# Optimization experiments

Measured on AMD Instinct MI355X. Metric: run time of the kernel, lower is better.

Reference implementation:

```python
import jax, jax.numpy as jnp
import numpy as np

H = 64; H2 = 32; B = 256; NPART = 64
NP = B * NPART          # 16384 part nodes
PER_TF = 512            # torque/force nodes per graph
NT = B * PER_TF; NF = NT
E = 262144              # edges per edge type
L = 5; T = 4            # 4 main hetero layers + 1 actor layer; 4 edge types
NEG = 0.2; EPS = 1e-5


def _seg_softmax(e, seg, n):
    # softmax over entries sharing the same segment id (along axis 0)
    m = jax.lax.stop_gradient(jax.ops.segment_max(e, seg, num_segments=n))
    ex = jnp.exp(e - m[seg])
    s = jax.ops.segment_sum(ex, seg, num_segments=n)
    return ex / s[seg]


def _gat(x_s, x_d, es, ed, Ws, Wd, a_s, a_d, b, n_dst):
    # PyG GATConv, heads=1, add_self_loops=False, bipartite (x_src, x_dst)
    hs = x_s @ Ws                      # [Ns,H]
    hd = x_d @ Wd                      # [Nd,H]
    e = jax.nn.leaky_relu((hs @ a_s)[es] + (hd @ a_d)[ed], NEG)   # [E]
    al = _seg_softmax(e, ed, n_dst)                                # attn per dst neighborhood
    return jax.ops.segment_sum(al[:, None] * hs[es], ed, num_segments=n_dst) + b


def _hetero_layer(xp, xt, xf, edges, Ws, Wd, a_s, a_d, b):
    # to_hetero(aggr='sum'): one GATConv per edge type, sum into each dst type
    (pts, ptd), (tps, tpd), (pfs, pfd), (fps, fpd) = edges
    out_t = _gat(xp, xt, pts, ptd, Ws[0], Wd[0], a_s[0], a_d[0], b[0], xt.shape[0])
    out_p = (_gat(xt, xp, tps, tpd, Ws[1], Wd[1], a_s[1], a_d[1], b[1], xp.shape[0])
             + _gat(xf, xp, fps, fpd, Ws[3], Wd[3], a_s[3], a_d[3], b[3], xp.shape[0]))
    out_f = _gat(xp, xf, pfs, pfd, Ws[2], Wd[2], a_s[2], a_d[2], b[2], xf.shape[0])
    return out_p, out_t, out_f


def _pool(x):
    # MultiAggregation([max, min, mean]); segments are uniform -> reshape
    xr = x.reshape(B, -1, x.shape[-1])
    return jnp.concatenate([xr.max(1), xr.min(1), xr.mean(1)], axis=-1)


def reference(mass, part_state, torque_x, force_x,
              e_pt_src, e_pt_dst, e_tp_src, e_tp_dst,
              e_pf_src, e_pf_dst, e_fp_src, e_fp_dst,
              batch, part_id,
              emb_parts_W, emb_state, W_src, W_dst, a_src, a_dst, b_conv,
              ln_gamma, ln_beta, out_a_W, out_a_b,
              innet_W, innet_b, full_W, full_b, outnet_W, outnet_b):
    edges = ((e_pt_src, e_pt_dst), (e_tp_src, e_tp_dst),
             (e_pf_src, e_pf_dst), (e_fp_src, e_fp_dst))
    idx = part_state[:, 0] + 2 * part_state[:, 1]
    xp = jnp.concatenate([mass @ emb_parts_W, emb_state[idx]], axis=-1)  # [NP,H]
    xt, xf = torque_x, force_x
    for l in range(4):  # main hetero GAT, ReLU between layers, none after last
        xp, xt, xf = _hetero_layer(xp, xt, xf, edges,
                                   W_src[l], W_dst[l], a_src[l], a_dst[l], b_conv[l])
        if l < 3:
            xp, xt, xf = jax.nn.relu(xp), jax.nn.relu(xt), jax.nn.relu(xf)
    # actor: 1-layer hetero GAT (no activation)
    ap, at, af = _hetero_layer(xp, xt, xf, edges,
                               W_src[4], W_dst[4], a_src[4], a_dst[4], b_conv[4])
    # node LayerNorm
    mu = ap.mean(-1, keepdims=True)
    var = ((ap - mu) ** 2).mean(-1, keepdims=True)
    ra = (ap - mu) / jnp.sqrt(var + EPS) * ln_gamma + ln_beta
    ra = ra @ out_a_W + out_a_b                         # [NP,2]
    soft = _seg_softmax(ra, batch, B)                   # softmax per graph, per channel
    actions = jnp.zeros((B, 2, NPART), dtype=ra.dtype).at[batch, :, part_id].set(soft)
    actions = actions.reshape(B, 2 * NPART)
    rep = jnp.concatenate([_pool(xp), _pool(xt), _pool(xf)], axis=1)   # [B, 9H]
    repV = jax.nn.gelu(rep @ innet_W + innet_b, approximate=False)
    repV = jax.nn.gelu(repV @ full_W + full_b, approximate=False)
    V = jnp.tanh(repV @ outnet_W + outnet_b)            # [B,1]
    return actions, V


def setup_inputs():
    key = jax.random.key(0)
    ks = iter(jax.random.split(key, 40))
    f32 = jnp.float32
    inp = {}
    inp['mass'] = jax.random.uniform(next(ks), (NP, 1), dtype=f32)
    inp['part_state'] = jax.random.randint(next(ks), (NP, 2), 0, 2, dtype=jnp.int32)
    inp['torque_x'] = jax.random.normal(next(ks), (NT, H), dtype=f32)
    inp['force_x'] = jax.random.normal(next(ks), (NF, H), dtype=f32)
    for name, n in [('e_pt_src', NP), ('e_pt_dst', NT), ('e_tp_src', NT), ('e_tp_dst', NP),
                    ('e_pf_src', NP), ('e_pf_dst', NF), ('e_fp_src', NF), ('e_fp_dst', NP)]:
        inp[name] = jax.random.randint(next(ks), (E,), 0, n, dtype=jnp.int32)
    inp['batch'] = (jnp.arange(NP) // NPART).astype(jnp.int32)
    inp['part_id'] = (jnp.arange(NP) % NPART).astype(jnp.int32)
    s = 1.0 / np.sqrt(H)
    inp['emb_parts_W'] = jax.random.normal(next(ks), (1, H2), dtype=f32)
    inp['emb_state'] = jax.random.normal(next(ks), (4, H2), dtype=f32)
    inp['W_src'] = jax.random.normal(next(ks), (L, T, H, H), dtype=f32) * s
    inp['W_dst'] = jax.random.normal(next(ks), (L, T, H, H), dtype=f32) * s
    inp['a_src'] = jax.random.normal(next(ks), (L, T, H), dtype=f32) * s
    inp['a_dst'] = jax.random.normal(next(ks), (L, T, H), dtype=f32) * s
    inp['b_conv'] = jax.random.normal(next(ks), (L, T, H), dtype=f32) * 0.01
    inp['ln_gamma'] = jnp.ones((H,), dtype=f32)
    inp['ln_beta'] = jnp.zeros((H,), dtype=f32)
    inp['out_a_W'] = jax.random.normal(next(ks), (H, 2), dtype=f32) * s
    inp['out_a_b'] = jnp.zeros((2,), dtype=f32)
    inp['innet_W'] = jax.random.normal(next(ks), (9 * H, H), dtype=f32) / np.sqrt(9.0 * H)
    inp['innet_b'] = jnp.zeros((H,), dtype=f32)
    inp['full_W'] = jax.random.normal(next(ks), (H, H), dtype=f32) * s
    inp['full_b'] = jnp.zeros((H,), dtype=f32)
    inp['outnet_W'] = jax.random.normal(next(ks), (H, 1), dtype=f32) * s
    inp['outnet_b'] = jnp.zeros((1,), dtype=f32)
    return inp
```

## Files before the change

kernel.cpp:

```cpp
#include <hip/hip_runtime.h>
#include <math.h>

#define NP_ 16384
#define NT_ 131072
#define NF_ 131072
#define E_  262144
#define B_  256
#define NDTOT 294912
#define E4_  1048576

#define D0 0
#define D1 131072
#define D2 147456
#define D3 278528
#define S0 0
#define S1 16384
#define S2 147456
#define S3 163840

__device__ __forceinline__ float dot4(float4 a, float4 b) {
  return a.x * b.x + a.y * b.y + a.z * b.z + a.w * b.w;
}

__device__ __forceinline__ void gather2(
    int kb0, int ke0, float ad0, const float* __restrict__ aS0, const float* __restrict__ x0,
    int kb1, int ke1, float ad1, const float* __restrict__ aS1, const float* __restrict__ x1,
    const int* __restrict__ sortsrc, int q, int lanebase,
    float4* __restrict__ acc0o, float* __restrict__ si0o,
    float4* __restrict__ acc1o, float* __restrict__ si1o) {
  float4 acc0 = make_float4(0.f, 0.f, 0.f, 0.f);
  float4 acc1 = make_float4(0.f, 0.f, 0.f, 0.f);
  float m0 = -3e38f, m1 = -3e38f, sum0 = 0.f, sum1 = 0.f;
  int len = max(ke0 - kb0, ke1 - kb1);
  for (int c = 0; c < len; c += 16) {
    int k0 = kb0 + c + q, k1 = kb1 + c + q;
    int v0 = k0 < ke0, v1 = k1 < ke1;
    int sx0 = v0 ? sortsrc[k0] : 0;
    int sx1 = v1 ? sortsrc[k1] : 0;
    float e0 = -3e38f, e1 = -3e38f;
    if (v0) { float t = aS0[sx0] + ad0; e0 = t > 0.f ? t : 0.2f * t; }
    if (v1) { float t = aS1[sx1] + ad1; e1 = t > 0.f ? t : 0.2f * t; }
    float cm0 = e0, cm1 = e1;
#pragma unroll
    for (int off = 1; off < 16; off <<= 1) {
      cm0 = fmaxf(cm0, __shfl_xor(cm0, off));
      cm1 = fmaxf(cm1, __shfl_xor(cm1, off));
    }
    float mn0 = fmaxf(m0, cm0), mn1 = fmaxf(m1, cm1);
    float w0 = v0 ? __expf(e0 - mn0) : 0.f;
    float w1 = v1 ? __expf(e1 - mn1) : 0.f;
    float ws0 = w0, ws1 = w1;
#pragma unroll
    for (int off = 1; off < 16; off <<= 1) {
      ws0 += __shfl_xor(ws0, off);
      ws1 += __shfl_xor(ws1, off);
    }
    float r0 = __expf(m0 - mn0), r1 = __expf(m1 - mn1);
    sum0 = sum0 * r0 + ws0;
    sum1 = sum1 * r1 + ws1;
    acc0.x *= r0; acc0.y *= r0; acc0.z *= r0; acc0.w *= r0;
    acc1.x *= r1; acc1.y *= r1; acc1.z *= r1; acc1.w *= r1;
    int cnt0 = ke0 - (kb0 + c); cnt0 = cnt0 < 0 ? 0 : (cnt0 > 16 ? 16 : cnt0);
    int cnt1 = ke1 - (kb1 + c); cnt1 = cnt1 < 0 ? 0 : (cnt1 > 16 ? 16 : cnt1);
    int cmax = max(cnt0, cnt1);
    for (int i = 0; i < cmax; i += 4) {
      float wa0 = __shfl(w0, lanebase + i, 64);
      float wa1 = __shfl(w0, lanebase + i + 1, 64);
      float wa2 = __shfl(w0, lanebase + i + 2, 64);
      float wa3 = __shfl(w0, lanebase + i + 3, 64);
      int sa0 = __shfl(sx0, lanebase + i, 64);
      int sa1 = __shfl(sx0, lanebase + i + 1, 64);
      int sa2 = __shfl(sx0, lanebase + i + 2, 64);
      int sa3 = __shfl(sx0, lanebase + i + 3, 64);
      float wb0 = __shfl(w1, lanebase + i, 64);
      float wb1 = __shfl(w1, lanebase + i + 1, 64);
      float wb2 = __shfl(w1, lanebase + i + 2, 64);
      float wb3 = __shfl(w1, lanebase + i + 3, 64);
      int sb0 = __shfl(sx1, lanebase + i, 64);
      int sb1 = __shfl(sx1, lanebase + i + 1, 64);
      int sb2 = __shfl(sx1, lanebase + i + 2, 64);
      int sb3 = __shfl(sx1, lanebase + i + 3, 64);
      float4 xa0 = *(const float4*)(x0 + (size_t)sa0 * 64 + q * 4);
      float4 xa1 = *(const float4*)(x0 + (size_t)sa1 * 64 + q * 4);
      float4 xa2 = *(const float4*)(x0 + (size_t)sa2 * 64 + q * 4);
      float4 xa3 = *(const float4*)(x0 + (size_t)sa3 * 64 + q * 4);
      float4 xb0 = *(const float4*)(x1 + (size_t)sb0 * 64 + q * 4);
      float4 xb1 = *(const float4*)(x1 + (size_t)sb1 * 64 + q * 4);
      float4 xb2 = *(const float4*)(x1 + (size_t)sb2 * 64 + q * 4);
      float4 xb3 = *(const float4*)(x1 + (size_t)sb3 * 64 + q * 4);
      acc0.x += wa0 * xa0.x + wa1 * xa1.x + wa2 * xa2.x + wa3 * xa3.x;
      acc0.y += wa0 * xa0.y + wa1 * xa1.y + wa2 * xa2.y + wa3 * xa3.y;
      acc0.z += wa0 * xa0.z + wa1 * xa1.z + wa2 * xa2.z + wa3 * xa3.z;
      acc0.w += wa0 * xa0.w + wa1 * xa1.w + wa2 * xa2.w + wa3 * xa3.w;
      acc1.x += wb0 * xb0.x + wb1 * xb1.x + wb2 * xb2.x + wb3 * xb3.x;
      acc1.y += wb0 * xb0.y + wb1 * xb1.y + wb2 * xb2.y + wb3 * xb3.y;
      acc1.z += wb0 * xb0.z + wb1 * xb1.z + wb2 * xb2.z + wb3 * xb3.z;
      acc1.w += wb0 * xb0.w + wb1 * xb1.w + wb2 * xb2.w + wb3 * xb3.w;
    }
    m0 = mn0; m1 = mn1;
  }
  *si0o = (sum0 > 0.f) ? 1.f / sum0 : 0.f;
  *si1o = (sum1 > 0.f) ? 1.f / sum1 : 0.f;
  *acc0o = acc0;
  *acc1o = acc1;
}

__device__ __forceinline__ void gather4(
    int kbA, int keA, float adA,
    int kbB, int keB, float adB,
    int kbC, int keC, float adC,
    int kbD, int keD, float adD,
    const float* __restrict__ aS, const float* __restrict__ x,
    const int* __restrict__ sortsrc, int q, int lanebase,
    float4* accAo, float* siAo, float4* accBo, float* siBo,
    float4* accCo, float* siCo, float4* accDo, float* siDo) {
  float4 aA = make_float4(0.f, 0.f, 0.f, 0.f);
  float4 aB = aA, aC = aA, aDv = aA;
  float mA = -3e38f, mB = -3e38f, mC = -3e38f, mD = -3e38f;
  float sA = 0.f, sB = 0.f, sC = 0.f, sD = 0.f;
  int len = max(max(keA - kbA, keB - kbB), max(keC - kbC, keD - kbD));
  for (int c = 0; c < len; c += 16) {
    int kA = kbA + c + q, kB = kbB + c + q, kC = kbC + c + q, kD = kbD + c + q;
    int vA = kA < keA, vB = kB < keB, vC = kC < keC, vD = kD < keD;
    int iA = vA ? sortsrc[kA] : 0;
    int iB = vB ? sortsrc[kB] : 0;
    int iC = vC ? sortsrc[kC] : 0;
    int iD = vD ? sortsrc[kD] : 0;
    float eA = -3e38f, eB = -3e38f, eC = -3e38f, eD = -3e38f;
    if (vA) { float u = aS[iA] + adA; eA = u > 0.f ? u : 0.2f * u; }
    if (vB) { float u = aS[iB] + adB; eB = u > 0.f ? u : 0.2f * u; }
    if (vC) { float u = aS[iC] + adC; eC = u > 0.f ? u : 0.2f * u; }
    if (vD) { float u = aS[iD] + adD; eD = u > 0.f ? u : 0.2f * u; }
    float cA = eA, cB = eB, cC = eC, cD = eD;
#pragma unroll
    for (int off = 1; off < 16; off <<= 1) {
      cA = fmaxf(cA, __shfl_xor(cA, off));
      cB = fmaxf(cB, __shfl_xor(cB, off));
      cC = fmaxf(cC, __shfl_xor(cC, off));
      cD = fmaxf(cD, __shfl_xor(cD, off));
    }
    float nA = fmaxf(mA, cA), nB = fmaxf(mB, cB);
    float nC = fmaxf(mC, cC), nD = fmaxf(mD, cD);
    float wA = vA ? __expf(eA - nA) : 0.f;
    float wB = vB ? __expf(eB - nB) : 0.f;
    float wC = vC ? __expf(eC - nC) : 0.f;
    float wD = vD ? __expf(eD - nD) : 0.f;
    float uA = wA, uB = wB, uC = wC, uD = wD;
#pragma unroll
    for (int off = 1; off < 16; off <<= 1) {
      uA += __shfl_xor(uA, off);
      uB += __shfl_xor(uB, off);
      uC += __shfl_xor(uC, off);
      uD += __shfl_xor(uD, off);
    }
    float rA = __expf(mA - nA), rB = __expf(mB - nB);
    float rC = __expf(mC - nC), rD = __expf(mD - nD);
    sA = sA * rA + uA; sB = sB * rB + uB;
// ... 280 lines not shown
    pos = atomicAdd(&cur[d.z >> sh], 1); pairs[pos] = make_int2(d.z, s.z);
    pos = atomicAdd(&cur[d.w >> sh], 1); pairs[pos] = make_int2(d.w, s.w);
  }
}

__global__ __launch_bounds__(256) void k_build(const int2* __restrict__ pairs,
    const int* __restrict__ granBase, int* __restrict__ rowptr,
    int* __restrict__ sortsrc) {
  __shared__ int cnt[2048];
  __shared__ int psum[256];
  int g = blockIdx.x;
  int t = g >> 6, gg = g & 63;
  int rows = (t & 1) ? 256 : 2048;
  int rowLo = gg * rows;
  int csr0;
  if (t == 0) csr0 = D0 + rowLo;
  else if (t == 1) csr0 = D1 + rowLo;
  else if (t == 2) csr0 = D2 + rowLo;
  else csr0 = D3 + rowLo;
  int eb = granBase[g], ee = granBase[g + 1];
  int tid = threadIdx.x;
  for (int i = tid; i < rows; i += 256) cnt[i] = 0;
  __syncthreads();
  for (int i = eb + tid; i < ee; i += 256) {
    int2 p = pairs[i];
    atomicAdd(&cnt[p.x - rowLo], 1);
  }
  __syncthreads();
  int per = rows >> 8;
  int b0 = tid * per;
  int s = 0;
  for (int j = 0; j < per; j++) s += cnt[b0 + j];
  psum[tid] = s;
  __syncthreads();
  for (int off = 1; off < 256; off <<= 1) {
    int x = 0; if (tid >= off) x = psum[tid - off];
    __syncthreads(); psum[tid] += x; __syncthreads();
  }
  int run = psum[tid] - s;
  for (int j = 0; j < per; j++) {
    int v = cnt[b0 + j];
    cnt[b0 + j] = run;
    rowptr[csr0 + b0 + j] = eb + run;
    run += v;
  }
  __syncthreads();
  for (int i = eb + tid; i < ee; i += 256) {
    int2 p = pairs[i];
    int pos = eb + atomicAdd(&cnt[p.x - rowLo], 1);
    sortsrc[pos] = p.y;
  }
}

__global__ __launch_bounds__(256) void k_part(int l,
    const float* __restrict__ Wsrc, const float* __restrict__ bconv,
    const float* __restrict__ xt, const float* __restrict__ xf,
    const int* __restrict__ rowptr, const int* __restrict__ sortsrc,
    const float* __restrict__ aSrd, const float* __restrict__ aDrd,
    float* __restrict__ aSwr, float* __restrict__ aDwr,
    const float* __restrict__ wsas, const float* __restrict__ wdad,
    float* __restrict__ xpo, float* __restrict__ hs0n, float* __restrict__ hs2n,
    int relu, int writeHs, int writeXp,
    const float* __restrict__ gamma, const float* __restrict__ beta,
    const float* __restrict__ oaW, const float* __restrict__ oab,
    float* __restrict__ raOut) {
  __shared__ float WA[4096], WB[4096];
  int tid = threadIdx.x;
  int q = tid & 15;
  int lanebase = (tid & 63) & 48;
  int n = blockIdx.x * 16 + (tid >> 4);
  {
    const float4* W1g = (const float4*)(Wsrc + (size_t)(l * 4 + 1) * 4096);
    const float4* W3g = (const float4*)(Wsrc + (size_t)(l * 4 + 3) * 4096);
#pragma unroll
    for (int i = 0; i < 4; i++) {
      ((float4*)WA)[i * 256 + tid] = W1g[i * 256 + tid];
      ((float4*)WB)[i * 256 + tid] = W3g[i * 256 + tid];
    }
  }
  __syncthreads();

  int row1 = D1 + n, row3 = D3 + n;
  int kb1 = rowptr[row1], ke1 = rowptr[row1 + 1];
  int kb3 = rowptr[row3], ke3 = rowptr[row3 + 1];
  float4 accA, accB; float siA, siB;
  gather2(kb1, ke1, aDrd[row1], aSrd + S1, xt,
          kb3, ke3, aDrd[row3], aSrd + S3, xf,
          sortsrc, q, lanebase, &accA, &siA, &accB, &siB);
  accA.x *= siA; accA.y *= siA; accA.z *= siA; accA.w *= siA;
  accB.x *= siB; accB.y *= siB; accB.z *= siB; accB.w *= siB;

  float4 o;
  {
    float4 b1 = *(const float4*)(bconv + (size_t)(l * 4 + 1) * 64 + q * 4);
    float4 b3 = *(const float4*)(bconv + (size_t)(l * 4 + 3) * 64 + q * 4);
    o = make_float4(b1.x + b3.x, b1.y + b3.y, b1.z + b3.z, b1.w + b3.w);
  }
  const float4* WAc = (const float4*)WA;
  const float4* WBc = (const float4*)WB;
#pragma unroll 4
  for (int k4 = 0; k4 < 16; k4++) {
    float ax = __shfl(accA.x, lanebase + k4, 64);
    float ay = __shfl(accA.y, lanebase + k4, 64);
    float az = __shfl(accA.z, lanebase + k4, 64);
    float aw = __shfl(accA.w, lanebase + k4, 64);
    float bx = __shfl(accB.x, lanebase + k4, 64);
    float by = __shfl(accB.y, lanebase + k4, 64);
    float bz = __shfl(accB.z, lanebase + k4, 64);
    float bw = __shfl(accB.w, lanebase + k4, 64);
    float4 wa0 = WAc[(k4 * 4 + 0) * 16 + q];
    float4 wa1 = WAc[(k4 * 4 + 1) * 16 + q];
    float4 wa2 = WAc[(k4 * 4 + 2) * 16 + q];
    float4 wa3 = WAc[(k4 * 4 + 3) * 16 + q];
    float4 wb0 = WBc[(k4 * 4 + 0) * 16 + q];
    float4 wb1 = WBc[(k4 * 4 + 1) * 16 + q];
    float4 wb2 = WBc[(k4 * 4 + 2) * 16 + q];
    float4 wb3 = WBc[(k4 * 4 + 3) * 16 + q];
    o.x += ax * wa0.x + ay * wa1.x + az * wa2.x + aw * wa3.x
         + bx * wb0.x + by * wb1.x + bz * wb2.x + bw * wb3.x;
    o.y += ax * wa0.y + ay * wa1.y + az * wa2.y + aw * wa3.y
         + bx * wb0.y + by * wb1.y + bz * wb2.y + bw * wb3.y;
    o.z += ax * wa0.z + ay * wa1.z + az * wa2.z + aw * wa3.z
         + bx * wb0.z + by * wb1.z + bz * wb2.z + bw * wb3.z;
    o.w += ax * wa0.w + ay * wa1.w + az * wa2.w + aw * wa3.w
         + bx * wb0.w + by * wb1.w + bz * wb2.w + bw * wb3.w;
  }

  if (raOut) {
    float ssum = o.x + o.y + o.z + o.w;
#pragma unroll
    for (int off = 1; off < 16; off <<= 1) ssum += __shfl_xor(ssum, off);
    float mean = ssum * (1.f / 64.f);
    float dx = o.x - mean, dy = o.y - mean, dz = o.z - mean, dw = o.w - mean;
    float v2 = dx * dx + dy * dy + dz * dz + dw * dw;
#pragma unroll
    for (int off = 1; off < 16; off <<= 1) v2 += __shfl_xor(v2, off);
    float rstd = 1.f / sqrtf(v2 * (1.f / 64.f) + 1e-5f);
    float4 g4 = *(const float4*)(gamma + q * 4);
    float4 be4 = *(const float4*)(beta + q * 4);
    float y0 = dx * rstd * g4.x + be4.x;
    float y1 = dy * rstd * g4.y + be4.y;
    float y2 = dz * rstd * g4.z + be4.z;
    float y3 = dw * rstd * g4.w + be4.w;
// ... 19 lines not shown
  {
    float4 w0 = *(const float4*)(wsas + (size_t)((l + 1) * 4 + 0) * 64 + q * 4);
    float4 w2 = *(const float4*)(wsas + (size_t)((l + 1) * 4 + 2) * 64 + q * 4);
    float4 d1 = *(const float4*)(wdad + (size_t)((l + 1) * 4 + 1) * 64 + q * 4);
    float4 d3 = *(const float4*)(wdad + (size_t)((l + 1) * 4 + 3) * 64 + q * 4);
    float p0 = dot4(o, w0), p2 = dot4(o, w2), p1 = dot4(o, d1), p3 = dot4(o, d3);
#pragma unroll
    for (int off = 1; off < 16; off <<= 1) {
      p0 += __shfl_xor(p0, off); p2 += __shfl_xor(p2, off);
      p1 += __shfl_xor(p1, off); p3 += __shfl_xor(p3, off);
    }
    if (q == 0) { aSwr[S0 + n] = p0; aSwr[S2 + n] = p2; aDwr[D1 + n] = p1; aDwr[D3 + n] = p3; }
  }

  if (writeHs) {
    __syncthreads();
    {
      const float4* W0g = (const float4*)(Wsrc + (size_t)((l + 1) * 4 + 0) * 4096);
      const float4* W2g = (const float4*)(Wsrc + (size_t)((l + 1) * 4 + 2) * 4096);
#pragma unroll
      for (int i = 0; i < 4; i++) {
        ((float4*)WA)[i * 256 + tid] = W0g[i * 256 + tid];
        ((float4*)WB)[i * 256 + tid] = W2g[i * 256 + tid];
      }
    }
    __syncthreads();
    float4 h0 = make_float4(0.f, 0.f, 0.f, 0.f);
    float4 h2 = make_float4(0.f, 0.f, 0.f, 0.f);
#pragma unroll 4
    for (int k4 = 0; k4 < 16; k4++) {
      float ox = __shfl(o.x, lanebase + k4, 64);
      float oy = __shfl(o.y, lanebase + k4, 64);
      float oz = __shfl(o.z, lanebase + k4, 64);
      float ow = __shfl(o.w, lanebase + k4, 64);
      float4 a0 = WAc[(k4 * 4 + 0) * 16 + q];
      float4 a1 = WAc[(k4 * 4 + 1) * 16 + q];
      float4 a2 = WAc[(k4 * 4 + 2) * 16 + q];
      float4 a3 = WAc[(k4 * 4 + 3) * 16 + q];
      float4 c0 = WBc[(k4 * 4 + 0) * 16 + q];
      float4 c1 = WBc[(k4 * 4 + 1) * 16 + q];
      float4 c2 = WBc[(k4 * 4 + 2) * 16 + q];
      float4 c3 = WBc[(k4 * 4 + 3) * 16 + q];
      h0.x += ox * a0.x + oy * a1.x + oz * a2.x + ow * a3.x;
      h0.y += ox * a0.y + oy * a1.y + oz * a2.y + ow * a3.y;
      h0.z += ox * a0.z + oy * a1.z + oz * a2.z + ow * a3.z;
      h0.w += ox * a0.w + oy * a1.w + oz * a2.w + ow * a3.w;
      h2.x += ox * c0.x + oy * c1.x + oz * c2.x + ow * c3.x;
      h2.y += ox * c0.y + oy * c1.y + oz * c2.y + ow * c3.y;
      h2.z += ox * c0.z + oy * c1.z + oz * c2.z + ow * c3.z;
      h2.w += ox * c0.w + oy * c1.w + oz * c2.w + ow * c3.w;
    }
    *(float4*)(hs0n + (size_t)n * 64 + q * 4) = h0;
    *(float4*)(hs2n + (size_t)n * 64 + q * 4) = h2;
  }
}

__global__ __launch_bounds__(256) void k_tf(int l, const float* __restrict__ hs0,
    const float* __restrict__ hs2, const float* __restrict__ bconv,
    const int* __restrict__ rowptr, const int* __restrict__ sortsrc,
    const float* __restrict__ aSrd, const float* __restrict__ aDrd,
    float* __restrict__ aSwr, float* __restrict__ aDwr,
    const float* __restrict__ wsas, const float* __restrict__ wdad,
    float* __restrict__ xt, float* __restrict__ xf, int relu) {
  int tid = threadIdx.x;
  int q = tid & 15, slot = tid >> 4;
  int lanebase = (tid & 63) & 48;
  int b = blockIdx.x;
  int isF = (b >= 2048);
  int r0 = (isF ? b - 2048 : b) * 64 + slot;
  int csr = (isF ? D2 : D0) + r0;
  const float* hs = isF ? hs2 : hs0;
  const float* aSseg = aSrd + (isF ? S2 : S0);
  int t = isF ? 2 : 0;

  int kbA = rowptr[csr],      keA = rowptr[csr + 1];
  int kbB = rowptr[csr + 16], keB = rowptr[csr + 17];
  int kbC = rowptr[csr + 32], keC = rowptr[csr + 33];
  int kbD = rowptr[csr + 48], keD = rowptr[csr + 49];
  float4 aA, aB, aC, aD4; float sA, sB, sC, sD;
  gather4(kbA, keA, aDrd[csr],      kbB, keB, aDrd[csr + 16],
          kbC, keC, aDrd[csr + 32], kbD, keD, aDrd[csr + 48],
          aSseg, hs, sortsrc, q, lanebase,
          &aA, &sA, &aB, &sB, &aC, &sC, &aD4, &sD);

  float4 bias = *(const float4*)(bconv + (size_t)(l * 4 + t) * 64 + q * 4);
  float4 o0, o1, o2, o3;
  o0.x = aA.x * sA + bias.x; o0.y = aA.y * sA + bias.y;
  o0.z = aA.z * sA + bias.z; o0.w = aA.w * sA + bias.w;
  o1.x = aB.x * sB + bias.x; o1.y = aB.y * sB + bias.y;
  o1.z = aB.z * sB + bias.z; o1.w = aB.w * sB + bias.w;
  o2.x = aC.x * sC + bias.x; o2.y = aC.y * sC + bias.y;
  o2.z = aC.z * sC + bias.z; o2.w = aC.w * sC + bias.w;
  o3.x = aD4.x * sD + bias.x; o3.y = aD4.y * sD + bias.y;
  o3.z = aD4.z * sD + bias.z; o3.w = aD4.w * sD + bias.w;
  if (relu) {
    o0.x = fmaxf(o0.x, 0.f); o0.y = fmaxf(o0.y, 0.f); o0.z = fmaxf(o0.z, 0.f); o0.w = fmaxf(o0.w, 0.f);
    o1.x = fmaxf(o1.x, 0.f); o1.y = fmaxf(o1.y, 0.f); o1.z = fmaxf(o1.z, 0.f); o1.w = fmaxf(o1.w, 0.f);
    o2.x = fmaxf(o2.x, 0.f); o2.y = fmaxf(o2.y, 0.f); o2.z = fmaxf(o2.z, 0.f); o2.w = fmaxf(o2.w, 0.f);
    o3.x = fmaxf(o3.x, 0.f); o3.y = fmaxf(o3.y, 0.f); o3.z = fmaxf(o3.z, 0.f); o3.w = fmaxf(o3.w, 0.f);
  }
  float* xout = isF ? xf : xt;
  *(float4*)(xout + (size_t)r0 * 64 + q * 4) = o0;
  *(float4*)(xout + (size_t)(r0 + 16) * 64 + q * 4) = o1;
  *(float4*)(xout + (size_t)(r0 + 32) * 64 + q * 4) = o2;
  *(float4*)(xout + (size_t)(r0 + 48) * 64 + q * 4) = o3;

  int tsrc = isF ? 3 : 1, tdst = isF ? 2 : 0;
  float4 wsv = *(const float4*)(wsas + (size_t)((l + 1) * 4 + tsrc) * 64 + q * 4);
  float4 wdv = *(const float4*)(wdad + (size_t)((l + 1) * 4 + tdst) * 64 + q * 4);
  float pS0 = dot4(o0, wsv), pD0 = dot4(o0, wdv);
  float pS1 = dot4(o1, wsv), pD1 = dot4(o1, wdv);
  float pS2 = dot4(o2, wsv), pD2 = dot4(o2, wdv);
  float pS3 = dot4(o3, wsv), pD3 = dot4(o3, wdv);
#pragma unroll
  for (int off = 1; off < 16; off <<= 1) {
    pS0 += __shfl_xor(pS0, off); pD0 += __shfl_xor(pD0, off);
    pS1 += __shfl_xor(pS1, off); pD1 += __shfl_xor(pD1, off);
    pS2 += __shfl_xor(pS2, off); pD2 += __shfl_xor(pD2, off);
    pS3 += __shfl_xor(pS3, off); pD3 += __shfl_xor(pD3, off);
  }
  if (q == 0) {
    int sb = isF ? S3 : S1;
    int db = isF ? D2 : D0;
    aSwr[sb + r0]      = pS0; aDwr[db + r0]      = pD0;
    aSwr[sb + r0 + 16] = pS1; aDwr[db + r0 + 16] = pD1;
    aSwr[sb + r0 + 32] = pS2; aDwr[db + r0 + 32] = pD2;
    aSwr[sb + r0 + 48] = pS3; aDwr[db + r0 + 48] = pD3;
  }
}

__global__ __launch_bounds__(64) void k_actor(const float* __restrict__ ra,
                                              float* __restrict__ outp) {
  int g = blockIdx.x;
  int p = threadIdx.x;
  float2 rv = *(const float2*)(ra + (size_t)(g * 64 + p) * 2);
  float m0 = rv.x, m1 = rv.y;
  for (int off = 32; off > 0; off >>= 1) {
    m0 = fmaxf(m0, __shfl_xor(m0, off));
    m1 = fmaxf(m1, __shfl_xor(m1, off));
  }
  float e0 = __expf(rv.x - m0), e1 = __expf(rv.y - m1);
  float s0 = e0, s1 = e1;
  for (int off = 32; off > 0; off >>= 1) {
    s0 += __shfl_xor(s0, off);
    s1 += __shfl_xor(s1, off);
  }
  outp[g * 128 + p] = e0 / s0;
  outp[g * 128 + 64 + p] = e1 / s1;
}

__global__ __launch_bounds__(256) void k_pool(const float* __restrict__ xp,
    const float* __restrict__ xt, const float* __restrict__ xf,
    float* __restrict__ pool) {
  __shared__ float pmax[4][64], pmin[4][64], psum[4][64];
  int b = blockIdx.x;
  int g = b / 9, c = b % 9;
  int tid = threadIdx.x;
  int grp = tid >> 6, col = tid & 63;
  const float* src; int R;
  if (c == 0)      { src = xp + (size_t)g * 64 * 64; R = 64; }
  else if (c <= 4) { src = xt + ((size_t)g * 512 + (size_t)(c - 1) * 128) * 64; R = 128; }
  else             { src = xf + ((size_t)g * 512 + (size_t)(c - 5) * 128) * 64; R = 128; }
  float mx = -3e38f, mn = 3e38f, sm = 0.f;
  for (int r = grp; r < R; r += 4) {
    float v = src[(size_t)r * 64 + col];
    mx = fmaxf(mx, v); mn = fminf(mn, v); sm += v;
  }
  pmax[grp][col] = mx; pmin[grp][col] = mn; psum[grp][col] = sm;
  __syncthreads();
  if (grp == 0) {
    float M = fmaxf(fmaxf(pmax[0][col], pmax[1][col]), fmaxf(pmax[2][col], pmax[3][col]));
    float m = fminf(fminf(pmin[0][col], pmin[1][col]), fminf(pmin[2][col], pmin[3][col]));
    float S = psum[0][col] + psum[1][col] + psum[2][col] + psum[3][col];
    float* o = pool + ((size_t)(g * 9 + c) * 3) * 64;
    o[col] = M; o[64 + col] = m; o[128 + col] = S;
  }
}

__global__ __launch_bounds__(256) void k_vhead(const float* __restrict__ pool,
    const float* __restrict__ inW, const float* __restrict__ inb,
// ... 35 lines not shown
  if (tid < 64) {
    float s = red[tid] + red[64 + tid] + red[128 + tid] + red[192 + tid] + inb[tid];
    h1[tid] = 0.5f * s * (1.f + erff(s * ISQ2));
  }
  __syncthreads();
  if (tid < 64) {
    float s = fb[tid];
    for (int k = 0; k < 64; k++) s += h1[k] * fW[k * 64 + tid];
    float h2 = 0.5f * s * (1.f + erff(s * ISQ2));
    float p = h2 * oW[tid];
    for (int off = 32; off > 0; off >>= 1) p += __shfl_xor(p, off);
    if (tid == 0) outV[g] = tanhf(p + ob[0]);
  }
}

extern "C" void kernel_launch(void* const* d_in, const int* in_sizes, int n_in,
                              void* d_out, int out_size, void* d_ws, size_t ws_size,
                              hipStream_t stream) {
  (void)in_sizes; (void)n_in; (void)out_size; (void)ws_size;
  const float* mass = (const float*)d_in[0];
  const int*   ps   = (const int*)d_in[1];
  const float* torque_x = (const float*)d_in[2];
  const float* force_x  = (const float*)d_in[3];
  const int* ept_s = (const int*)d_in[4];  const int* ept_d = (const int*)d_in[5];
  const int* etp_s = (const int*)d_in[6];  const int* etp_d = (const int*)d_in[7];
  const int* epf_s = (const int*)d_in[8];  const int* epf_d = (const int*)d_in[9];
  const int* efp_s = (const int*)d_in[10]; const int* efp_d = (const int*)d_in[11];
  const float* embW  = (const float*)d_in[14];
  const float* embS  = (const float*)d_in[15];
  const float* Wsrc  = (const float*)d_in[16];
  const float* Wdst  = (const float*)d_in[17];
  const float* asrc  = (const float*)d_in[18];
  const float* adst  = (const float*)d_in[19];
  const float* bconv = (const float*)d_in[20];
  const float* gamma = (const float*)d_in[21];
  const float* beta  = (const float*)d_in[22];
  const float* oaW   = (const float*)d_in[23];
  const float* oab   = (const float*)d_in[24];
  const float* inW   = (const float*)d_in[25];
  const float* inb   = (const float*)d_in[26];
  const float* fW    = (const float*)d_in[27];
  const float* fb    = (const float*)d_in[28];
  const float* oW    = (const float*)d_in[29];
  const float* ob    = (const float*)d_in[30];

  char* base = (char*)d_ws;
  size_t off = 0;
  auto alloc = [&](size_t bytes) -> void* {
    void* r = base + off;
    off = (off + bytes + 255) & ~(size_t)255;
    return r;
  };
  float* xp  = (float*)alloc((size_t)NP_ * 64 * 4);
  float* xt  = (float*)alloc((size_t)NT_ * 64 * 4);
  float* xf  = (float*)alloc((size_t)NF_ * 64 * 4);
  float* hs0b[2], *hs2b[2];
  hs0b[0] = (float*)alloc((size_t)NP_ * 64 * 4);
  hs0b[1] = (float*)alloc((size_t)NP_ * 64 * 4);
  hs2b[0] = (float*)alloc((size_t)NP_ * 64 * 4);
  hs2b[1] = (float*)alloc((size_t)NP_ * 64 * 4);
  float* aSb[2], *aDb[2];
  aSb[0] = (float*)alloc((size_t)NDTOT * 4);
  aSb[1] = (float*)alloc((size_t)NDTOT * 4);
  aDb[0] = (float*)alloc((size_t)NDTOT * 4);
  aDb[1] = (float*)alloc((size_t)NDTOT * 4);
  float* wsas = (float*)alloc(1280 * 4);
  float* wdad = (float*)alloc(1280 * 4);
  float* pool = (float*)alloc((size_t)B_ * 9 * 3 * 64 * 4);
  float* ra   = (float*)alloc((size_t)NP_ * 2 * 4);
  int* rowptr = (int*)alloc((size_t)(NDTOT + 1) * 4);
  int* sortsrc = (int*)alloc((size_t)E4_ * 4);
  int2* pairs  = (int2*)alloc((size_t)E4_ * 8);
  int* counts  = (int*)alloc(16384 * 4);
  int* cbase   = (int*)alloc(16384 * 4);
  int* granBase = (int*)alloc(257 * 4);

  k_wa<<<40, 64, 0, stream>>>(Wsrc, Wdst, asrc, adst, wsas, wdad);
  k_build_xp<<<NP_ / 16, 256, 0, stream>>>(mass, ps, embW, embS, Wsrc, wsas, wdad,
                                           hs0b[0], hs2b[0], aSb[0], aDb[0]);
  k_init_dots<<<(NT_ + NF_) / 16, 256, 0, stream>>>(torque_x, force_x,
                                                    wsas, wdad, aSb[0], aDb[0]);
  k_count<<<256, 256, 0, stream>>>(ept_d, etp_d, epf_d, efp_d, counts);
  k_bases<<<1, 256, 0, stream>>>(counts, cbase, granBase, rowptr);
  k_place<<<256, 256, 0, stream>>>(ept_d, ept_s, etp_d, etp_s, epf_d, epf_s,
                                   efp_d, efp_s, cbase, pairs);
  k_build<<<256, 256, 0, stream>>>(pairs, granBase, rowptr, sortsrc);

  for (int l = 0; l < 5; l++) {
    int ri = l & 1, wi = (l + 1) & 1;
    int relu = (l < 3) ? 1 : 0;
    const float* xtr = (l == 0) ? torque_x : xt;
    const float* xfr = (l == 0) ? force_x : xf;
    k_part<<<NP_ / 16, 256, 0, stream>>>(l, Wsrc, bconv, xtr, xfr,
                                         rowptr, sortsrc,
                                         aSb[ri], aDb[ri], aSb[wi], aDb[wi],
                                         wsas, wdad, xp,
                                         hs0b[(l + 1) & 1], hs2b[(l + 1) & 1],
                                         relu, (l < 3) ? 1 : 0, (l == 3) ? 1 : 0,
                                         gamma, beta, oaW, oab,
                                         (l == 4) ? ra : (float*)nullptr);
    if (l < 4)
      k_tf<<<(NT_ + NF_) / 64, 256, 0, stream>>>(l, hs0b[l & 1], hs2b[l & 1], bconv,
                                                 rowptr, sortsrc,
                                                 aSb[ri], aDb[ri], aSb[wi], aDb[wi],
                                                 wsas, wdad, xt, xf, relu);
  }

  float* outp = (float*)d_out;
  k_actor<<<B_, 64, 0, stream>>>(ra, outp);
  k_pool<<<B_ * 9, 256, 0, stream>>>(xp, xt, xf, pool);
  k_vhead<<<B_, 256, 0, stream>>>(pool, inW, inb, fW, fb, oW, ob, outp + B_ * 128);
}
```

Before: 603.6 us.

## Merge part-node gathers with torque/force layer into one kernel, split part transform

The per-layer schedule is restructured. The part-node attention gathers (two edge types) now run as extra blocks inside a merged kernel together with the torque/force gathers. Each edge type gets its own 16-lane group rather than a paired gather2. A separate k_xform kernel then loads the aggregates and does the dense transform. xt/xf are double-buffered so the merged kernel can read the old features while writing new ones, and the aggregates reuse the pairs buffer. The intent is to fill the GPU with both gather workloads concurrently and reduce load imbalance, at the cost of an extra aggregate round-trip through memory.

```diff
diff --git a/kernel.cpp b/kernel.cpp
--- a/kernel.cpp
+++ b/kernel.cpp
@@ -22,87 +22,61 @@
   return a.x * b.x + a.y * b.y + a.z * b.z + a.w * b.w;
 }
 
-__device__ __forceinline__ void gather2(
-    int kb0, int ke0, float ad0, const float* __restrict__ aS0, const float* __restrict__ x0,
-    int kb1, int ke1, float ad1, const float* __restrict__ aS1, const float* __restrict__ x1,
-    const int* __restrict__ sortsrc, int q, int lanebase,
-    float4* __restrict__ acc0o, float* __restrict__ si0o,
-    float4* __restrict__ acc1o, float* __restrict__ si1o) {
-  float4 acc0 = make_float4(0.f, 0.f, 0.f, 0.f);
-  float4 acc1 = make_float4(0.f, 0.f, 0.f, 0.f);
-  float m0 = -3e38f, m1 = -3e38f, sum0 = 0.f, sum1 = 0.f;
-  int len = max(ke0 - kb0, ke1 - kb1);
-  for (int c = 0; c < len; c += 16) {
-    int k0 = kb0 + c + q, k1 = kb1 + c + q;
-    int v0 = k0 < ke0, v1 = k1 < ke1;
-    int sx0 = v0 ? sortsrc[k0] : 0;
-    int sx1 = v1 ? sortsrc[k1] : 0;
-    float e0 = -3e38f, e1 = -3e38f;
-    if (v0) { float t = aS0[sx0] + ad0; e0 = t > 0.f ? t : 0.2f * t; }
-    if (v1) { float t = aS1[sx1] + ad1; e1 = t > 0.f ? t : 0.2f * t; }
-    float cm0 = e0, cm1 = e1;
-#pragma unroll
-    for (int off = 1; off < 16; off <<= 1) {
-      cm0 = fmaxf(cm0, __shfl_xor(cm0, off));
-      cm1 = fmaxf(cm1, __shfl_xor(cm1, off));
-    }
-    float mn0 = fmaxf(m0, cm0), mn1 = fmaxf(m1, cm1);
-    float w0 = v0 ? __expf(e0 - mn0) : 0.f;
-    float w1 = v1 ? __expf(e1 - mn1) : 0.f;
-    float ws0 = w0, ws1 = w1;
-#pragma unroll
-    for (int off = 1; off < 16; off <<= 1) {
-      ws0 += __shfl_xor(ws0, off);
-      ws1 += __shfl_xor(ws1, off);
-    }
-    float r0 = __expf(m0 - mn0), r1 = __expf(m1 - mn1);
-    sum0 = sum0 * r0 + ws0;
-    sum1 = sum1 * r1 + ws1;
-    acc0.x *= r0; acc0.y *= r0; acc0.z *= r0; acc0.w *= r0;
-    acc1.x *= r1; acc1.y *= r1; acc1.z *= r1; acc1.w *= r1;
-    int cnt0 = ke0 - (kb0 + c); cnt0 = cnt0 < 0 ? 0 : (cnt0 > 16 ? 16 : cnt0);
-    int cnt1 = ke1 - (kb1 + c); cnt1 = cnt1 < 0 ? 0 : (cnt1 > 16 ? 16 : cnt1);
-    int cmax = max(cnt0, cnt1);
-    for (int i = 0; i < cmax; i += 4) {
-      float wa0 = __shfl(w0, lanebase + i, 64);
-      float wa1 = __shfl(w0, lanebase + i + 1, 64);
-      float wa2 = __shfl(w0, lanebase + i + 2, 64);
-      float wa3 = __shfl(w0, lanebase + i + 3, 64);
-      int sa0 = __shfl(sx0, lanebase + i, 64);
-      int sa1 = __shfl(sx0, lanebase + i + 1, 64);
-      int sa2 = __shfl(sx0, lanebase + i + 2, 64);
-      int sa3 = __shfl(sx0, lanebase + i + 3, 64);
-      float wb0 = __shfl(w1, lanebase + i, 64);
-      float wb1 = __shfl(w1, lanebase + i + 1, 64);
-      float wb2 = __shfl(w1, lanebase + i + 2, 64);
-      float wb3 = __shfl(w1, lanebase + i + 3, 64);
-      int sb0 = __shfl(sx1, lanebase + i, 64);
-      int sb1 = __shfl(sx1, lanebase + i + 1, 64);
-      int sb2 = __shfl(sx1, lanebase + i + 2, 64);
-      int sb3 = __shfl(sx1, lanebase + i + 3, 64);
-      float4 xa0 = *(const float4*)(x0 + (size_t)sa0 * 64 + q * 4);
-      float4 xa1 = *(const float4*)(x0 + (size_t)sa1 * 64 + q * 4);
-      float4 xa2 = *(const float4*)(x0 + (size_t)sa2 * 64 + q * 4);
-      float4 xa3 = *(const float4*)(x0 + (size_t)sa3 * 64 + q * 4);
-      float4 xb0 = *(const float4*)(x1 + (size_t)sb0 * 64 + q * 4);
-      float4 xb1 = *(const float4*)(x1 + (size_t)sb1 * 64 + q * 4);
-      float4 xb2 = *(const float4*)(x1 + (size_t)sb2 * 64 + q * 4);
-      float4 xb3 = *(const float4*)(x1 + (size_t)sb3 * 64 + q * 4);
-      acc0.x += wa0 * xa0.x + wa1 * xa1.x + wa2 * xa2.x + wa3 * xa3.x;
-      acc0.y += wa0 * xa0.y + wa1 * xa1.y + wa2 * xa2.y + wa3 * xa3.y;
-      acc0.z += wa0 * xa0.z + wa1 * xa1.z + wa2 * xa2.z + wa3 * xa3.z;
-      acc0.w += wa0 * xa0.w + wa1 * xa1.w + wa2 * xa2.w + wa3 * xa3.w;
-      acc1.x += wb0 * xb0.x + wb1 * xb1.x + wb2 * xb2.x + wb3 * xb3.x;
-      acc1.y += wb0 * xb0.y + wb1 * xb1.y + wb2 * xb2.y + wb3 * xb3.y;
-      acc1.z += wb0 * xb0.z + wb1 * xb1.z + wb2 * xb2.z + wb3 * xb3.z;
-      acc1.w += wb0 * xb0.w + wb1 * xb1.w + wb2 * xb2.w + wb3 * xb3.w;
-    }
-    m0 = mn0; m1 = mn1;
-  }
-  *si0o = (sum0 > 0.f) ? 1.f / sum0 : 0.f;
-  *si1o = (sum1 > 0.f) ? 1.f / sum1 : 0.f;
-  *acc0o = acc0;
-  *acc1o = acc1;
+__device__ __forceinline__ float4 gather_row(int kb, int ke, float ad,
+    const int* __restrict__ sortsrc, const float* __restrict__ aS_seg,
+    const float* __restrict__ xsrc, int q, int lanebase, float* si_out) {
+  float4 acc = make_float4(0.f, 0.f, 0.f, 0.f);
+  float m = -3e38f, ssum = 0.f;
+  for (int base = kb; base < ke; base += 16) {
+    int k = base + q;
+    int valid = (k < ke);
+    int sidx = valid ? sortsrc[k] : 0;
+    float e = -3e38f;
+    if (valid) {
+      e = aS_seg[sidx] + ad;
+      e = e > 0.f ? e : 0.2f * e;
+    }
+    float cm = e;
+#pragma unroll
+    for (int off = 1; off < 16; off <<= 1) cm = fmaxf(cm, __shfl_xor(cm, off));
+    float mn = fmaxf(m, cm);
+    float w = valid ? __expf(e - mn) : 0.f;
+    float ws = w;
+#pragma unroll
+    for (int off = 1; off < 16; off <<= 1) ws += __shfl_xor(ws, off);
+    float r = __expf(m - mn);
+    ssum = ssum * r + ws;
+    acc.x *= r; acc.y *= r; acc.z *= r; acc.w *= r;
+    int cnt = min(16, ke - base);
+    int i = 0;
+    for (; i + 4 <= cnt; i += 4) {
+      float w0 = __shfl(w, lanebase + i, 64);
+      float w1 = __shfl(w, lanebase + i + 1, 64);
+      float w2 = __shfl(w, lanebase + i + 2, 64);
+      float w3 = __shfl(w, lanebase + i + 3, 64);
+      int s0 = __shfl(sidx, lanebase + i, 64);
+      int s1 = __shfl(sidx, lanebase + i + 1, 64);
+      int s2 = __shfl(sidx, lanebase + i + 2, 64);
+      int s3 = __shfl(sidx, lanebase + i + 3, 64);
+      float4 x0 = *(const float4*)(xsrc + (size_t)s0 * 64 + q * 4);
+      float4 x1 = *(const float4*)(xsrc + (size_t)s1 * 64 + q * 4);
+      float4 x2 = *(const float4*)(xsrc + (size_t)s2 * 64 + q * 4);
+      float4 x3 = *(const float4*)(xsrc + (size_t)s3 * 64 + q * 4);
+      acc.x += w0 * x0.x + w1 * x1.x + w2 * x2.x + w3 * x3.x;
+      acc.y += w0 * x0.y + w1 * x1.y + w2 * x2.y + w3 * x3.y;
+      acc.z += w0 * x0.z + w1 * x1.z + w2 * x2.z + w3 * x3.z;
+      acc.w += w0 * x0.w + w1 * x1.w + w2 * x2.w + w3 * x3.w;
+    }
+    for (; i < cnt; i++) {
+      float wi = __shfl(w, lanebase + i, 64);
+      int si = __shfl(sidx, lanebase + i, 64);
+      float4 xv = *(const float4*)(xsrc + (size_t)si * 64 + q * 4);
+      acc.x += wi * xv.x; acc.y += wi * xv.y; acc.z += wi * xv.z; acc.w += wi * xv.w;
+    }
+    m = mn;
+  }
+  *si_out = (ssum > 0.f) ? 1.f / ssum : 0.f;
+  return acc;
 }
 
 __device__ __forceinline__ void gather4(
@@ -489,11 +463,112 @@
   }
 }
 
-__global__ __launch_bounds__(256) void k_part(int l,
-    const float* __restrict__ Wsrc, const float* __restrict__ bconv,
-    const float* __restrict__ xt, const float* __restrict__ xf,
+__global__ __launch_bounds__(256) void k_layer(int l,
+    const float* __restrict__ xt_old, const float* __restrict__ xf_old,
+    const float* __restrict__ hs0, const float* __restrict__ hs2,
+    const float* __restrict__ bconv,
     const int* __restrict__ rowptr, const int* __restrict__ sortsrc,
     const float* __restrict__ aSrd, const float* __restrict__ aDrd,
+    float* __restrict__ aSwr, float* __restrict__ aDwr,
+    const float* __restrict__ wsas, const float* __restrict__ wdad,
+    float* __restrict__ agg1, float* __restrict__ agg3,
+    float* __restrict__ xt_new, float* __restrict__ xf_new,
+    int relu, int hasTf) {
+  int bid = blockIdx.x;
+  int tid = threadIdx.x;
+  int q = tid & 15;
+  int lanebase = (tid & 63) & 48;
+
+  int isPart, pg = 0, tg = 0;
+  if (!hasTf) { isPart = 1; pg = bid; }
+  else {
+    int g = bid / 3, r = bid - g * 3;
+    if (r == 2) { isPart = 1; pg = g; }
+    else        { isPart = 0; tg = g * 2 + r; }
+  }
+
+  if (isPart) {
+    int half = (tid >> 4) & 1;
+    int n = pg * 8 + (tid >> 5);
+    int row = (half ? D3 : D1) + n;
+    const float* xsrc = half ? xf_old : xt_old;
+    const float* aSseg = aSrd + (half ? S3 : S1);
+    int kb = rowptr[row], ke = rowptr[row + 1];
+    float si;
+    float4 acc = gather_row(kb, ke, aDrd[row], sortsrc, aSseg, xsrc, q, lanebase, &si);
+    acc.x *= si; acc.y *= si; acc.z *= si; acc.w *= si;
+    float* dst = half ? agg3 : agg1;
+    *(float4*)(dst + (size_t)n * 64 + q * 4) = acc;
+    return;
+  }
+
+  int slot = tid >> 4;
+  int isF = (tg >= 2048);
+  int r0 = (isF ? tg - 2048 : tg) * 64 + slot;
+  int csr = (isF ? D2 : D0) + r0;
+  const float* hs = isF ? hs2 : hs0;
+  const float* aSseg = aSrd + (isF ? S2 : S0);
+  int t = isF ? 2 : 0;
+
+  int kbA = rowptr[csr],      keA = rowptr[csr + 1];
+  int kbB = rowptr[csr + 16], keB = rowptr[csr + 17];
+  int kbC = rowptr[csr + 32], keC = rowptr[csr + 33];
+  int kbD = rowptr[csr + 48], keD = rowptr[csr + 49];
+  float4 aA, aB, aC, aD4; float sA, sB, sC, sD;
+  gather4(kbA, keA, aDrd[csr],      kbB, keB, aDrd[csr + 16],
+          kbC, keC, aDrd[csr + 32], kbD, keD, aDrd[csr + 48],
+          aSseg, hs, sortsrc, q, lanebase,
+          &aA, &sA, &aB, &sB, &aC, &sC, &aD4, &sD);
+
+  float4 bias = *(const float4*)(bconv + (size_t)(l * 4 + t) * 64 + q * 4);
+  float4 o0, o1, o2, o3;
+  o0.x = aA.x * sA + bias.x; o0.y = aA.y * sA + bias.y;
+  o0.z = aA.z * sA + bias.z; o0.w = aA.w * sA + bias.w;
+  o1.x = aB.x * sB + bias.x; o1.y = aB.y * sB + bias.y;
+  o1.z = aB.z * sB + bias.z; o1.w = aB.w * sB + bias.w;
+  o2.x = aC.x * sC + bias.x; o2.y = aC.y * sC + bias.y;
+  o2.z = aC.z * sC + bias.z; o2.w = aC.w * sC + bias.w;
+  o3.x = aD4.x * sD + bias.x; o3.y = aD4.y * sD + bias.y;
+  o3.z = aD4.z * sD + bias.z; o3.w = aD4.w * sD + bias.w;
+  if (relu) {
+    o0.x = fmaxf(o0.x, 0.f); o0.y = fmaxf(o0.y, 0.f); o0.z = fmaxf(o0.z, 0.f); o0.w = fmaxf(o0.w, 0.f);
+    o1.x = fmaxf(o1.x, 0.f); o1.y = fmaxf(o1.y, 0.f); o1.z = fmaxf(o1.z, 0.f); o1.w = fmaxf(o1.w, 0.f);
+    o2.x = fmaxf(o2.x, 0.f); o2.y = fmaxf(o2.y, 0.f); o2.z = fmaxf(o2.z, 0.f); o2.w = fmaxf(o2.w, 0.f);
+    o3.x = fmaxf(o3.x, 0.f); o3.y = fmaxf(o3.y, 0.f); o3.z = fmaxf(o3.z, 0.f); o3.w = fmaxf(o3.w, 0.f);
+  }
+  float* xout = isF ? xf_new : xt_new;
+  *(float4*)(xout + (size_t)r0 * 64 + q * 4) = o0;
+  *(float4*)(xout + (size_t)(r0 + 16) * 64 + q * 4) = o1;
+  *(float4*)(xout + (size_t)(r0 + 32) * 64 + q * 4) = o2;
+  *(float4*)(xout + (size_t)(r0 + 48) * 64 + q * 4) = o3;
+
+  int tsrc = isF ? 3 : 1, tdst = isF ? 2 : 0;
+  float4 wsv = *(const float4*)(wsas + (size_t)((l + 1) * 4 + tsrc) * 64 + q * 4);
+  float4 wdv = *(const float4*)(wdad + (size_t)((l + 1) * 4 + tdst) * 64 + q * 4);
+  float pS0 = dot4(o0, wsv), pD0 = dot4(o0, wdv);
+  float pS1 = dot4(o1, wsv), pD1 = dot4(o1, wdv);
+  float pS2 = dot4(o2, wsv), pD2 = dot4(o2, wdv);
+  float pS3 = dot4(o3, wsv), pD3 = dot4(o3, wdv);
+#pragma unroll
+  for (int off = 1; off < 16; off <<= 1) {
+    pS0 += __shfl_xor(pS0, off); pD0 += __shfl_xor(pD0, off);
+    pS1 += __shfl_xor(pS1, off); pD1 += __shfl_xor(pD1, off);
+    pS2 += __shfl_xor(pS2, off); pD2 += __shfl_xor(pD2, off);
+    pS3 += __shfl_xor(pS3, off); pD3 += __shfl_xor(pD3, off);
+  }
+  if (q == 0) {
+    int sb = isF ? S3 : S1;
+    int db = isF ? D2 : D0;
+    aSwr[sb + r0]      = pS0; aDwr[db + r0]      = pD0;
+    aSwr[sb + r0 + 16] = pS1; aDwr[db + r0 + 16] = pD1;
+    aSwr[sb + r0 + 32] = pS2; aDwr[db + r0 + 32] = pD2;
+    aSwr[sb + r0 + 48] = pS3; aDwr[db + r0 + 48] = pD3;
+  }
+}
+
+__global__ __launch_bounds__(256) void k_xform(int l,
+    const float* __restrict__ Wsrc, const float* __restrict__ bconv,
+    const float* __restrict__ agg1, const float* __restrict__ agg3,
     float* __restrict__ aSwr, float* __restrict__ aDwr,
     const float* __restrict__ wsas, const float* __restrict__ wdad,
     float* __restrict__ xpo, float* __restrict__ hs0n, float* __restrict__ hs2n,
@@ -515,17 +590,9 @@
       ((float4*)WB)[i * 256 + tid] = W3g[i * 256 + tid];
     }
   }
-  __syncthreads();
-
-  int row1 = D1 + n, row3 = D3 + n;
-  int kb1 = rowptr[row1], ke1 = rowptr[row1 + 1];
-  int kb3 = rowptr[row3], ke3 = rowptr[row3 + 1];
-  float4 accA, accB; float siA, siB;
-  gather2(kb1, ke1, aDrd[row1], aSrd + S1, xt,
-          kb3, ke3, aDrd[row3], aSrd + S3, xf,
-          sortsrc, q, lanebase, &accA, &siA, &accB, &siB);
-  accA.x *= siA; accA.y *= siA; accA.z *= siA; accA.w *= siA;
-  accB.x *= siB; accB.y *= siB; accB.z *= siB; accB.w *= siB;
+  float4 accA = *(const float4*)(agg1 + (size_t)n * 64 + q * 4);
+  float4 accB = *(const float4*)(agg3 + (size_t)n * 64 + q * 4);
+  __syncthreads();
 
   float4 o;
   {
@@ -651,80 +718,6 @@
     }
     *(float4*)(hs0n + (size_t)n * 64 + q * 4) = h0;
     *(float4*)(hs2n + (size_t)n * 64 + q * 4) = h2;
-  }
-}
-
-__global__ __launch_bounds__(256) void k_tf(int l, const float* __restrict__ hs0,
-    const float* __restrict__ hs2, const float* __restrict__ bconv,
-    const int* __restrict__ rowptr, const int* __restrict__ sortsrc,
-    const float* __restrict__ aSrd, const float* __restrict__ aDrd,
-    float* __restrict__ aSwr, float* __restrict__ aDwr,
-    const float* __restrict__ wsas, const float* __restrict__ wdad,
-    float* __restrict__ xt, float* __restrict__ xf, int relu) {
-  int tid = threadIdx.x;
-  int q = tid & 15, slot = tid >> 4;
-  int lanebase = (tid & 63) & 48;
-  int b = blockIdx.x;
-  int isF = (b >= 2048);
-  int r0 = (isF ? b - 2048 : b) * 64 + slot;
-  int csr = (isF ? D2 : D0) + r0;
-  const float* hs = isF ? hs2 : hs0;
-  const float* aSseg = aSrd + (isF ? S2 : S0);
-  int t = isF ? 2 : 0;
-
-  int kbA = rowptr[csr],      keA = rowptr[csr + 1];
-  int kbB = rowptr[csr + 16], keB = rowptr[csr + 17];
-  int kbC = rowptr[csr + 32], keC = rowptr[csr + 33];
-  int kbD = rowptr[csr + 48], keD = rowptr[csr + 49];
-  float4 aA, aB, aC, aD4; float sA, sB, sC, sD;
-  gather4(kbA, keA, aDrd[csr],      kbB, keB, aDrd[csr + 16],
-          kbC, keC, aDrd[csr + 32], kbD, keD, aDrd[csr + 48],
-          aSseg, hs, sortsrc, q, lanebase,
-          &aA, &sA, &aB, &sB, &aC, &sC, &aD4, &sD);
-
-  float4 bias = *(const float4*)(bconv + (size_t)(l * 4 + t) * 64 + q * 4);
-  float4 o0, o1, o2, o3;
-  o0.x = aA.x * sA + bias.x; o0.y = aA.y * sA + bias.y;
-  o0.z = aA.z * sA + bias.z; o0.w = aA.w * sA + bias.w;
-  o1.x = aB.x * sB + bias.x; o1.y = aB.y * sB + bias.y;
-  o1.z = aB.z * sB + bias.z; o1.w = aB.w * sB + bias.w;
-  o2.x = aC.x * sC + bias.x; o2.y = aC.y * sC + bias.y;
-  o2.z = aC.z * sC + bias.z; o2.w = aC.w * sC + bias.w;
-  o3.x = aD4.x * sD + bias.x; o3.y = aD4.y * sD + bias.y;
-  o3.z = aD4.z * sD + bias.z; o3.w = aD4.w * sD + bias.w;
-  if (relu) {
-    o0.x = fmaxf(o0.x, 0.f); o0.y = fmaxf(o0.y, 0.f); o0.z = fmaxf(o0.z, 0.f); o0.w = fmaxf(o0.w, 0.f);
-    o1.x = fmaxf(o1.x, 0.f); o1.y = fmaxf(o1.y, 0.f); o1.z = fmaxf(o1.z, 0.f); o1.w = fmaxf(o1.w, 0.f);
-    o2.x = fmaxf(o2.x, 0.f); o2.y = fmaxf(o2.y, 0.f); o2.z = fmaxf(o2.z, 0.f); o2.w = fmaxf(o2.w, 0.f);
-    o3.x = fmaxf(o3.x, 0.f); o3.y = fmaxf(o3.y, 0.f); o3.z = fmaxf(o3.z, 0.f); o3.w = fmaxf(o3.w, 0.f);
-  }
-  float* xout = isF ? xf : xt;
-  *(float4*)(xout + (size_t)r0 * 64 + q * 4) = o0;
-  *(float4*)(xout + (size_t)(r0 + 16) * 64 + q * 4) = o1;
-  *(float4*)(xout + (size_t)(r0 + 32) * 64 + q * 4) = o2;
-  *(float4*)(xout + (size_t)(r0 + 48) * 64 + q * 4) = o3;
-
-  int tsrc = isF ? 3 : 1, tdst = isF ? 2 : 0;
-  float4 wsv = *(const float4*)(wsas + (size_t)((l + 1) * 4 + tsrc) * 64 + q * 4);
-  float4 wdv = *(const float4*)(wdad + (size_t)((l + 1) * 4 + tdst) * 64 + q * 4);
-  float pS0 = dot4(o0, wsv), pD0 = dot4(o0, wdv);
-  float pS1 = dot4(o1, wsv), pD1 = dot4(o1, wdv);
-  float pS2 = dot4(o2, wsv), pD2 = dot4(o2, wdv);
-  float pS3 = dot4(o3, wsv), pD3 = dot4(o3, wdv);
-#pragma unroll
-  for (int off = 1; off < 16; off <<= 1) {
-    pS0 += __shfl_xor(pS0, off); pD0 += __shfl_xor(pD0, off);
-    pS1 += __shfl_xor(pS1, off); pD1 += __shfl_xor(pD1, off);
-    pS2 += __shfl_xor(pS2, off); pD2 += __shfl_xor(pD2, off);
-    pS3 += __shfl_xor(pS3, off); pD3 += __shfl_xor(pD3, off);
-  }
-  if (q == 0) {
-    int sb = isF ? S3 : S1;
-    int db = isF ? D2 : D0;
-    aSwr[sb + r0]      = pS0; aDwr[db + r0]      = pD0;
-    aSwr[sb + r0 + 16] = pS1; aDwr[db + r0 + 16] = pD1;
-    aSwr[sb + r0 + 32] = pS2; aDwr[db + r0 + 32] = pD2;
-    aSwr[sb + r0 + 48] = pS3; aDwr[db + r0 + 48] = pD3;
   }
 }
 
@@ -866,8 +859,11 @@
     return r;
   };
   float* xp  = (float*)alloc((size_t)NP_ * 64 * 4);
-  float* xt  = (float*)alloc((size_t)NT_ * 64 * 4);
-  float* xf  = (float*)alloc((size_t)NF_ * 64 * 4);
+  float* xtb[2], *xfb[2];
+  xtb[0] = (float*)alloc((size_t)NT_ * 64 * 4);
+  xtb[1] = (float*)alloc((size_t)NT_ * 64 * 4);
+  xfb[0] = (float*)alloc((size_t)NF_ * 64 * 4);
+  xfb[1] = (float*)alloc((size_t)NF_ * 64 * 4);
   float* hs0b[2], *hs2b[2];
   hs0b[0] = (float*)alloc((size_t)NP_ * 64 * 4);
   hs0b[1] = (float*)alloc((size_t)NP_ * 64 * 4);
@@ -888,6 +884,8 @@
   int* counts  = (int*)alloc(16384 * 4);
   int* cbase   = (int*)alloc(16384 * 4);
   int* granBase = (int*)alloc(257 * 4);
+  float* agg1 = (float*)pairs;
+  float* agg3 = agg1 + (size_t)NP_ * 64;
 
   k_wa<<<40, 64, 0, stream>>>(Wsrc, Wdst, asrc, adst, wsas, wdad);
   k_build_xp<<<NP_ / 16, 256, 0, stream>>>(mass, ps, embW, embS, Wsrc, wsas, wdad,
@@ -903,25 +901,28 @@
   for (int l = 0; l < 5; l++) {
     int ri = l & 1, wi = (l + 1) & 1;
     int relu = (l < 3) ? 1 : 0;
-    const float* xtr = (l == 0) ? torque_x : xt;
-    const float* xfr = (l == 0) ? force_x : xf;
-    k_part<<<NP_ / 16, 256, 0, stream>>>(l, Wsrc, bconv, xtr, xfr,
-                                         rowptr, sortsrc,
-                                         aSb[ri], aDb[ri], aSb[wi], aDb[wi],
-                                         wsas, wdad, xp,
-                                         hs0b[(l + 1) & 1], hs2b[(l + 1) & 1],
-                                         relu, (l < 3) ? 1 : 0, (l == 3) ? 1 : 0,
-                                         gamma, beta, oaW, oab,
-                                         (l == 4) ? ra : (float*)nullptr);
-    if (l < 4)
-      k_tf<<<(NT_ + NF_) / 64, 256, 0, stream>>>(l, hs0b[l & 1], hs2b[l & 1], bconv,
-                                                 rowptr, sortsrc,
-                                                 aSb[ri], aDb[ri], aSb[wi], aDb[wi],
-                                                 wsas, wdad, xt, xf, relu);
+    const float* xt_old = (l == 0) ? torque_x : xtb[(l + 1) & 1];
+    const float* xf_old = (l == 0) ? force_x : xfb[(l + 1) & 1];
+    float* xt_new = xtb[l & 1];
+    float* xf_new = xfb[l & 1];
+    int hasTf = (l < 4) ? 1 : 0;
+    int grid = hasTf ? (NP_ / 8 + (NT_ + NF_) / 64) : (NP_ / 8);
+    k_layer<<<grid, 256, 0, stream>>>(l, xt_old, xf_old,
+                                      hs0b[l & 1], hs2b[l & 1], bconv,
+                                      rowptr, sortsrc,
+                                      aSb[ri], aDb[ri], aSb[wi], aDb[wi],
+                                      wsas, wdad, agg1, agg3,
+                                      xt_new, xf_new, relu, hasTf);
+    k_xform<<<NP_ / 16, 256, 0, stream>>>(l, Wsrc, bconv, agg1, agg3,
+                                          aSb[wi], aDb[wi], wsas, wdad,
+                                          xp, hs0b[(l + 1) & 1], hs2b[(l + 1) & 1],
+                                          relu, (l < 3) ? 1 : 0, (l == 3) ? 1 : 0,
+                                          gamma, beta, oaW, oab,
+                                          (l == 4) ? ra : (float*)nullptr);
   }
 
   float* outp = (float*)d_out;
   k_actor<<<B_, 64, 0, stream>>>(ra, outp);
-  k_pool<<<B_ * 9, 256, 0, stream>>>(xp, xt, xf, pool);
+  k_pool<<<B_ * 9, 256, 0, stream>>>(xp, xtb[1], xfb[1], pool);
   k_vhead<<<B_, 256, 0, stream>>>(pool, inW, inb, fW, fb, oW, ob, outp + B_ * 128);
 }
```

Measured after the change: 608.4 us. No clear change (+0.8%).
